# Optimization experiments

Measured on AMD Instinct MI355X. Metric: run time of the kernel, lower is better.

The kernel has to match this reference:

```python
import jax, jax.numpy as jnp
import numpy as np
import math

B, W, D, H, K = 32, 512, 512, 8, 64
DH = D // H

def _rms(x, s, eps=1e-6):
    return x / jnp.sqrt(jnp.mean(x * x, axis=-1, keepdims=True) + eps) * s

def _l2n(x):
    return x / (jnp.linalg.norm(x, axis=-1, keepdims=True) + 1e-6)

def _rope(x, fc):
    b, t, h, d = x.shape
    xc = jax.lax.complex(x[..., 0::2], x[..., 1::2])
    xr = xc * fc
    return jnp.stack([xr.real, xr.imag], axis=-1).reshape(b, t, h, d)

def setup_inputs() -> dict:
    key = jax.random.key(0)
    ks = jax.random.split(key, 24)
    n = lambda i, s: jax.random.normal(ks[i], s, jnp.float32) * 0.02
    return {
        'x': jax.random.normal(ks[0], (B, W, D), jnp.float32),
        'epi_keys': _l2n(jax.random.normal(ks[1], (B, K, D), jnp.float32)),
        'epi_vals': jax.random.normal(ks[2], (B, K, D), jnp.float32),
        'epi_age': jax.random.uniform(ks[3], (B, K), jnp.float32, 0.0, 10.0),
        'epi_strength': jax.random.uniform(ks[4], (B, K), jnp.float32, 0.01, 1.0),
        'pos_idx': jnp.arange(W, dtype=jnp.int32),
        'rms1': jnp.ones((D,), jnp.float32), 'rms_kv': jnp.ones((D,), jnp.float32),
        'rms2': jnp.ones((D,), jnp.float32), 'rms_read': jnp.ones((D,), jnp.float32),
        'Wq': n(5, (D, D)), 'bq': jnp.zeros((D,), jnp.float32),
        'Wk': n(6, (D, D)), 'bk': jnp.zeros((D,), jnp.float32),
        'Wv': n(7, (D, D)), 'bv': jnp.zeros((D,), jnp.float32),
        'Wo': n(8, (D, D)), 'bo': jnp.zeros((D,), jnp.float32),
        'W1': n(9, (D, 8 * D)), 'W2': n(10, (4 * D, D)),
        'Wwk': n(11, (D, D)), 'bwk': jnp.zeros((D,), jnp.float32),
        'Wwv': n(12, (D, D)), 'bwv': jnp.zeros((D,), jnp.float32),
        'Wws': n(13, (D, 1)), 'bws': jnp.zeros((1,), jnp.float32),
        'Wg1': n(14, (D + 2, D)), 'bg1': jnp.zeros((D,), jnp.float32),
        'Wg2': n(15, (D, 1)), 'bg2': jnp.zeros((1,), jnp.float32),
    }

def _cell(x, epi_keys, epi_vals, epi_age, epi_strength, pos_idx,
          rms1, rms_kv, rms2, rms_read, Wq, bq, Wk, bk, Wv, bv, Wo, bo,
          W1, W2, Wwk, bwk, Wwv, bwv, Wws, bws, Wg1, bg1, Wg2, bg2):
    Bc, T, Dc = x.shape
    # RoPE freqs at absolute window positions (slice_freqs_cis)
    freqs = 1.0 / (10000.0 ** (jnp.arange(0, DH, 2, dtype=jnp.float32) / DH))  # (DH/2,)
    ang = pos_idx.astype(jnp.float32)[:, None] * freqs[None, :]               # (T, DH/2)
    fc = jax.lax.complex(jnp.cos(ang), jnp.sin(ang))[None, :, None, :]        # (1,T,1,DH/2)
    # --- windowed causal RoPE attention (TransformerBlock) ---
    nx, nkv = _rms(x, rms1), _rms(x, rms_kv)
    q = _rope((nx @ Wq + bq).reshape(Bc, T, H, DH), fc)
    k = _rope((nkv @ Wk + bk).reshape(Bc, T, H, DH), fc)
    v = (nkv @ Wv + bv).reshape(Bc, T, H, DH)
    att = jnp.einsum('bthd,bshd->bhts', q, k) / math.sqrt(DH)
    causal = jnp.tril(jnp.ones((T, T), bool))
    att = jnp.where(causal[None, None], att, -1e9)
    p = jax.nn.softmax(att, axis=-1)
    o = jnp.einsum('bhts,bshd->bthd', p, v).reshape(Bc, T, Dc)
    h1 = x + (o @ Wo + bo)
    gv = _rms(h1, rms2) @ W1
    g, val = jnp.split(gv, 2, axis=-1)
    h2 = h1 + (jax.nn.silu(g) * val) @ W2                                     # (B,T,D)
    # --- window summary query ---
    q_win = jnp.mean(h2, axis=1)                                              # (B,D)
    # --- EpisodicSlotReader ---
    qn = _l2n(q_win)
    kn = _l2n(epi_keys)
    sim_r = jnp.sum(kn * qn[:, None, :], axis=-1)                             # (B,K)
    logits = sim_r + 0.5 * jnp.log(jnp.clip(epi_strength, 0.001, 1e9)) - 0.02 * epi_age
    logits = logits + ((epi_strength > 0.001).astype(jnp.float32) - 1.0) * 1000.0
    w_read = jax.nn.softmax(logits, axis=-1)
    read = _rms(jnp.sum(w_read[:, :, None] * epi_vals, axis=1), rms_read)     # (B,D)
    # --- write projections ---
    write_key = q_win @ Wwk + bwk
    write_val = q_win @ Wwv + bwv
    ws = jnp.clip(jax.nn.sigmoid(q_win @ Wws + bws), 0.0, 1.0)                # (B,1)
    # --- EpisodicSlotWriter (ST top-1 competitive write) ---
    wk_n = _l2n(write_key)
    sim_w = jnp.sum(kn * wk_n[:, None, :], axis=-1)                           # (B,K)
    soft = jax.nn.softmax(sim_w * 50.0, axis=-1)
    hard = jax.nn.one_hot(jnp.argmax(soft, axis=-1), K, dtype=jnp.float32)
    write_w = jax.lax.stop_gradient(hard - soft) + soft
    eff = write_w * ws * 0.5                                                  # (B,K)
    re = eff[:, :, None]
    keys_new = _l2n((1.0 - re) * epi_keys + re * write_key[:, None, :])
    vals_new = (1.0 - re) * epi_vals + re * write_val[:, None, :]
    age_new = (epi_age + 1.0) * (1.0 - write_w)
    sn = epi_strength * 0.995
    sn = jnp.clip(sn + write_w * ws * (1.0 - sn), 0.001, 1.0)
    best_sim = jnp.max(sim_w, axis=-1)                                        # (B,)
    # --- MemoryRecallGate ---
    novelty = (1.0 - best_sim)[:, None]
    xg = jnp.concatenate([q_win, ws, novelty], axis=-1)                       # (B,D+2)
    gate = jax.nn.sigmoid(jax.nn.silu(xg @ Wg1 + bg1) @ Wg2 + bg2)            # (B,1)
    out = h2 + (gate * read)[:, None, :]
    return out, keys_new, vals_new, age_new, sn, gate

def reference(x, epi_keys, epi_vals, epi_age, epi_strength, pos_idx,
              rms1, rms_kv, rms2, rms_read, Wq, bq, Wk, bk, Wv, bv, Wo, bo,
              W1, W2, Wwk, bwk, Wwv, bwv, Wws, bws, Wg1, bg1, Wg2, bg2):
    return _cell(x, epi_keys, epi_vals, epi_age, epi_strength, pos_idx,
                 rms1, rms_kv, rms2, rms_read, Wq, bq, Wk, bk, Wv, bv, Wo, bo,
                 W1, W2, Wwk, bwk, Wwv, bwv, Wws, bws, Wg1, bg1, Wg2, bg2)
```

## Files before the change

### kernel.cpp

```cpp
#include <hip/hip_runtime.h>


#define DEVI __device__ __forceinline__
typedef unsigned short u16;
typedef unsigned int   u32;
typedef __bf16 v8bf __attribute__((ext_vector_type(8)));
typedef float  v4f  __attribute__((ext_vector_type(4)));

DEVI float bf2f(u16 u) { u32 v = ((u32)u) << 16; return __builtin_bit_cast(float, v); }
DEVI u16 f2bf(float f) {
  u32 x = __builtin_bit_cast(u32, f);
  u32 r = x + 0x7fffu + ((x >> 16) & 1u);
  return (u16)(r >> 16);
}
DEVI uint4 pack8(const float* f) {
  u32 a[4];
#pragma unroll
  for (int i = 0; i < 4; ++i)
    a[i] = (u32)f2bf(f[2*i]) | ((u32)f2bf(f[2*i+1]) << 16);
  uint4 v; v.x = a[0]; v.y = a[1]; v.z = a[2]; v.w = a[3]; return v;
}
DEVI void ld8f(const float* p, float* f) {
  float4 a = *(const float4*)p, b = *(const float4*)(p + 4);
  f[0]=a.x; f[1]=a.y; f[2]=a.z; f[3]=a.w; f[4]=b.x; f[5]=b.y; f[6]=b.z; f[7]=b.w;
}
DEVI void st8f(float* p, const float* f) {
  *(float4*)p       = make_float4(f[0], f[1], f[2], f[3]);
  *(float4*)(p + 4) = make_float4(f[4], f[5], f[6], f[7]);
}
DEVI v8bf ldfrag(const u16* p) { return __builtin_bit_cast(v8bf, *(const uint4*)p); }

DEVI void async16(const u16* g, u16* l) {
  __builtin_amdgcn_global_load_lds(
      (const __attribute__((address_space(1))) void*)g,
      (__attribute__((address_space(3))) void*)l, 16, 0, 0);
}

DEVI float wave_sum64(float v) {
  v += __shfl_xor(v, 1);  v += __shfl_xor(v, 2);  v += __shfl_xor(v, 4);
  v += __shfl_xor(v, 8);  v += __shfl_xor(v, 16); v += __shfl_xor(v, 32);
  return v;
}

__device__ float block_sum256(float v, float* sred) {
  v = wave_sum64(v);
  int w = threadIdx.x >> 6;
  __syncthreads();
  if ((threadIdx.x & 63) == 0) sred[w] = v;
  __syncthreads();
  return sred[0] + sred[1] + sred[2] + sred[3];
}

__global__ __launch_bounds__(256) void transpose_all_k(
    const float* __restrict__ Wq, const float* __restrict__ Wk,
    const float* __restrict__ Wv, const float* __restrict__ Wo,
    const float* __restrict__ W1, const float* __restrict__ W2,
    const float* __restrict__ rms1, const float* __restrict__ rms_kv,
    const float* __restrict__ rms2, u16* __restrict__ WTqkv,
    u16* __restrict__ WTo, u16* __restrict__ WT1, u16* __restrict__ WT2,
    const float* __restrict__ bq, const float* __restrict__ bk,
    const float* __restrict__ bv, float* __restrict__ bias_qkv) {
  int id = blockIdx.x;
  if (id >= 4096) {
    int j = (id - 4096) * 256 + threadIdx.x;
    bias_qkv[j] = j < 512 ? bq[j] : (j < 1024 ? bk[j - 512] : bv[j - 1024]);
    return;
  }
  const float* in; const float* scale; u16* outp; int R, C, bx, by;
  if (id < 256)       { in=Wq; scale=rms1;   outp=WTqkv;            R=512;  C=512;  int l=id;       bx=l&15;  by=l>>4; }
  else if (id < 512)  { in=Wk; scale=rms_kv; outp=WTqkv+512*512;    R=512;  C=512;  int l=id-256;   bx=l&15;  by=l>>4; }
  else if (id < 768)  { in=Wv; scale=rms_kv; outp=WTqkv+1024*512;   R=512;  C=512;  int l=id-512;   bx=l&15;  by=l>>4; }
  else if (id < 1024) { in=Wo; scale=nullptr;outp=WTo;              R=512;  C=512;  int l=id-768;   bx=l&15;  by=l>>4; }
  else if (id < 3072) { in=W1; scale=rms2;   outp=WT1;              R=512;  C=4096; int l=id-1024;  bx=l&127; by=l>>7; }
  else                { in=W2; scale=nullptr;outp=WT2;              R=2048; C=512;  int l=id-3072;  bx=l&15;  by=l>>4; }
  __shared__ u16 t[32][33];
  int c0 = bx * 32, r0 = by * 32;
  int lc = threadIdx.x & 31, lr = threadIdx.x >> 5;
  for (int rr = lr; rr < 32; rr += 8) {
    float v = in[(size_t)(r0 + rr) * C + c0 + lc];
    if (scale) v *= scale[r0 + rr];
    t[rr][lc] = f2bf(v);
  }
  __syncthreads();
  for (int rr = lr; rr < 32; rr += 8)
    outp[(size_t)(c0 + rr) * R + r0 + lc] = t[lc][rr];
}

__global__ __launch_bounds__(256) void rms_k(const float* __restrict__ x,
                                             u16* __restrict__ o1) {
  int w = threadIdx.x >> 6, lane = threadIdx.x & 63;
  size_t row = (size_t)blockIdx.x * 4 + w;
  float xf[8]; ld8f(x + row * 512 + lane * 8, xf);
  float ss = 0.f;
#pragma unroll
  for (int i = 0; i < 8; ++i) ss += xf[i] * xf[i];
  ss = wave_sum64(ss);
  float inv = rsqrtf(ss * (1.f / 512.f) + 1e-6f);
  float of[8];
#pragma unroll
  for (int i = 0; i < 8; ++i) of[i] = xf[i] * inv;
  *(uint4*)(o1 + row * 512 + lane * 8) = pack8(of);
}

__global__ __launch_bounds__(256) void gemm128_k(const u16* __restrict__ A,
                                                 const u16* __restrict__ BT,
                                                 const float* __restrict__ bias,
                                                 const float* __restrict__ resf,
                                                 u16* __restrict__ outb,
                                                 float* __restrict__ outf,
                                                 int N, int Kd) {
  __shared__ u16 As[128 * 64];
  __shared__ u16 Bs[128 * 64];
  int tid = threadIdx.x;
  int w = tid >> 6, lane = tid & 63;
  int m = lane & 15, quad = lane >> 4;
  int wm = w >> 1, wn = w & 1;
  int bm = blockIdx.x, bn = blockIdx.y;
  v4f acc[4][4] = {};
  const int gswz = ((lane & 7) ^ (lane >> 3)) * 8;
  const u16* Ag = A + (size_t)(bm * 128 + w * 32 + (lane >> 3)) * Kd + gswz;
  const u16* Bg = BT + (size_t)(bn * 128 + w * 32 + (lane >> 3)) * Kd + gswz;
  u16* Al = &As[w * 32 * 64];
  u16* Bl = &Bs[w * 32 * 64];
  const int rsw = (m & 7) * 8;
  for (int k0 = 0; k0 < Kd; k0 += 64) {
#pragma unroll
    for (int it = 0; it < 4; ++it) {
      async16(Ag + (size_t)it * 8 * Kd + k0, Al + it * 8 * 64);
      async16(Bg + (size_t)it * 8 * Kd + k0, Bl + it * 8 * 64);
    }
    __syncthreads();
#pragma unroll
    for (int kk = 0; kk < 2; ++kk) {
      v8bf af[4], bfr[4];
#pragma unroll
      for (int i = 0; i < 4; ++i)
        af[i] = ldfrag(&As[(wm * 64 + i * 16 + m) * 64 +
                           ((kk * 32 + quad * 8) ^ rsw)]);
#pragma unroll
      for (int j = 0; j < 4; ++j)
        bfr[j] = ldfrag(&Bs[(wn * 64 + j * 16 + m) * 64 +
                            ((kk * 32 + quad * 8) ^ rsw)]);
#pragma unroll
      for (int i = 0; i < 4; ++i)
#pragma unroll
        for (int j = 0; j < 4; ++j)
          acc[i][j] = __builtin_amdgcn_mfma_f32_16x16x32_bf16(af[i], bfr[j],
                                                              acc[i][j], 0, 0, 0);
    }
    __syncthreads();
  }
#pragma unroll
  for (int i = 0; i < 4; ++i) {
    int grow0 = bm * 128 + wm * 64 + i * 16 + quad * 4;
#pragma unroll
    for (int j = 0; j < 4; ++j) {
      int gcol = bn * 128 + wn * 64 + j * 16 + m;
      float bv = bias ? bias[gcol] : 0.f;
#pragma unroll
      for (int rr = 0; rr < 4; ++rr) {
        size_t idx = (size_t)(grow0 + rr) * N + gcol;
        float v = acc[i][j][rr] + bv;
        if (resf) v += resf[idx];
        if (outb) outb[idx] = f2bf(v);
        else      outf[idx] = v;
      }
    }
  }
}

__global__ __launch_bounds__(256) void mlp1_k(const u16* __restrict__ A,
                                              const u16* __restrict__ W1T,
                                              u16* __restrict__ out) {
  __shared__ u16 As[128 * 64];
  __shared__ u16 Bgs[64 * 64];
  __shared__ u16 Bvs[64 * 64];
  const int Kd = 512;
  int tid = threadIdx.x;
  int w = tid >> 6, lane = tid & 63;
  int m = lane & 15, quad = lane >> 4;
  int bm = blockIdx.x, bn = blockIdx.y;
  v4f accg[2][4] = {}, accv[2][4] = {};
  const int gswz = ((lane & 7) ^ (lane >> 3)) * 8;
  const u16* Ag  = A + (size_t)(bm * 128 + w * 32 + (lane >> 3)) * Kd + gswz;
  const u16* Bgp = W1T + (size_t)(bn * 64 + w * 16 + (lane >> 3)) * Kd + gswz;
  const u16* Bvp = W1T + (size_t)(2048 + bn * 64 + w * 16 + (lane >> 3)) * Kd + gswz;
  u16* Al  = &As[w * 32 * 64];
  u16* Bgl = &Bgs[w * 16 * 64];
  u16* Bvl = &Bvs[w * 16 * 64];
  const int rsw = (m & 7) * 8;
  for (int k0 = 0; k0 < Kd; k0 += 64) {
#pragma unroll
    for (int it = 0; it < 4; ++it)
      async16(Ag + (size_t)it * 8 * Kd + k0, Al + it * 8 * 64);
#pragma unroll
    for (int it = 0; it < 2; ++it) {
      async16(Bgp + (size_t)it * 8 * Kd + k0, Bgl + it * 8 * 64);
      async16(Bvp + (size_t)it * 8 * Kd + k0, Bvl + it * 8 * 64);
    }
    __syncthreads();
#pragma unroll
    for (int kk = 0; kk < 2; ++kk) {
      v8bf af[2], bg[4], bv[4];
#pragma unroll
      for (int i = 0; i < 2; ++i)
        af[i] = ldfrag(&As[(w * 32 + i * 16 + m) * 64 +
                           ((kk * 32 + quad * 8) ^ rsw)]);
#pragma unroll
      for (int j = 0; j < 4; ++j) {
        bg[j] = ldfrag(&Bgs[(j * 16 + m) * 64 + ((kk * 32 + quad * 8) ^ rsw)]);
        bv[j] = ldfrag(&Bvs[(j * 16 + m) * 64 + ((kk * 32 + quad * 8) ^ rsw)]);
      }
#pragma unroll
      for (int i = 0; i < 2; ++i)
#pragma unroll
        for (int j = 0; j < 4; ++j) {
          accg[i][j] = __builtin_amdgcn_mfma_f32_16x16x32_bf16(af[i], bg[j],
                                                               accg[i][j], 0, 0, 0);
          accv[i][j] = __builtin_amdgcn_mfma_f32_16x16x32_bf16(af[i], bv[j],
                                                               accv[i][j], 0, 0, 0);
        }
    }
    __syncthreads();
  }
#pragma unroll
  for (int i = 0; i < 2; ++i) {
    int grow0 = bm * 128 + w * 32 + i * 16 + quad * 4;
#pragma unroll
    for (int j = 0; j < 4; ++j) {
      int gcol = bn * 64 + j * 16 + m;
#pragma unroll
      for (int rr = 0; rr < 4; ++rr) {
        float g = accg[i][j][rr];
        float sv = g / (1.f + __expf(-g));
        out[(size_t)(grow0 + rr) * 2048 + gcol] = f2bf(sv * accv[i][j][rr]);
      }
    }
  }
}

__global__ __launch_bounds__(256) void rope_qk_k(u16* __restrict__ qkv,
                                                 const int* __restrict__ pos) {
  int pid = blockIdx.x * 256 + threadIdx.x;
  int half = pid >> 22;
  int sub = pid & 0x3FFFFF;
  int row = sub >> 8;
  int pr = sub & 255;
  int tt = row & 511;
  int col2 = half * 512 + pr * 2;
  int f = pr & 31;
  float freq = exp2f(-0.41524101186f * (float)f);
  float ang = (float)pos[tt] * freq;
  float sv, cv;
  sincosf(ang, &sv, &cv);
  u16* p = qkv + (size_t)row * 1536 + col2;
  u32 v = *(u32*)p;
  float e = bf2f((u16)(v & 0xffffu)), o = bf2f((u16)(v >> 16));
  float ne = e * cv - o * sv;
  float no = e * sv + o * cv;
  *(u32*)p = (u32)f2bf(ne) | ((u32)f2bf(no) << 16);
}

__global__ __launch_bounds__(1024) void attn_k(const u16* __restrict__ qkv,
                                               u16* __restrict__ og) {
  __shared__ u16 Ks[512 * 64];
  __shared__ u16 Vt[64 * 512];
  __shared__ u16 Ps[16][16 * 40];
  int tid = threadIdx.x;
  int w = tid >> 6, lane = tid & 63;
  int m = lane & 15, quad = lane >> 4;
  int bh = blockIdx.x;
  int b = bh >> 3, h = bh & 7;
  const size_t qbase = (size_t)b * 512 * 1536 + h * 64;
  const size_t obase = (size_t)b * 512 * 512 + h * 64;
  const u16* kbase = qkv + (size_t)b * 512 * 1536 + 512 + h * 64;
  const u16* vbase = kbase + 512;

  {
    int d8 = (tid & 7) * 8;
    for (int s = tid >> 3; s < 512; s += 128) {
      uint4 t4 = *(const uint4*)(kbase + (size_t)s * 1536 + d8);
      *(uint4*)&Ks[s * 64 + (d8 ^ ((s & 7) * 8))] = t4;
    }
  }
  {
    int d = tid & 63, sw = (d & 7) * 8;
    for (int s = tid >> 6; s < 512; s += 16)
      Vt[d * 512 + (s ^ sw)] = vbase[(size_t)s * 1536 + d];
  }
  __syncthreads();

  for (int rep = 0; rep < 2; ++rep) {
    int qt = rep == 0 ? w : 31 - w;
    int tb = qt * 16;
    const u16* qp = qkv + qbase + (size_t)(tb + m) * 1536;
    v8bf aq0 = ldfrag(qp + quad * 8);
    v8bf aq1 = ldfrag(qp + 32 + quad * 8);
    v4f acc[4] = {};
    float mr[4], lr_[4];
#pragma unroll
    for (int rr = 0; rr < 4; ++rr) { mr[rr] = -1.0e30f; lr_[rr] = 0.f; }
    int swz = (m & 7) * 8;

    for (int st2 = 0; st2 <= qt; st2 += 2) {
      int srA = st2 * 16 + m;
      v8bf ka0 = ldfrag(&Ks[srA * 64 + ((quad * 8) ^ swz)]);
      v8bf ka1 = ldfrag(&Ks[srA * 64 + ((32 + quad * 8) ^ swz)]);
      v4f s4a = {};
      __builtin_amdgcn_s_setprio(1);
      s4a = __builtin_amdgcn_mfma_f32_16x16x32_bf16(aq0, ka0, s4a, 0, 0, 0);
      s4a = __builtin_amdgcn_mfma_f32_16x16x32_bf16(aq1, ka1, s4a, 0, 0, 0);
      __builtin_amdgcn_s_setprio(0);
      bool haveB = (st2 + 1 <= qt);
      v4f s4b = {};
      if (haveB) {
        int srB = srA + 16;
        v8bf kb0 = ldfrag(&Ks[srB * 64 + ((quad * 8) ^ swz)]);
        v8bf kb1 = ldfrag(&Ks[srB * 64 + ((32 + quad * 8) ^ swz)]);
        __builtin_amdgcn_s_setprio(1);
        s4b = __builtin_amdgcn_mfma_f32_16x16x32_bf16(aq0, kb0, s4b, 0, 0, 0);
        s4b = __builtin_amdgcn_mfma_f32_16x16x32_bf16(aq1, kb1, s4b, 0, 0, 0);
        __builtin_amdgcn_s_setprio(0);
      }
      float sca[4], scb[4];
#pragma unroll
      for (int rr = 0; rr < 4; ++rr) {
        int rowt = tb + quad * 4 + rr;
        sca[rr] = s4a[rr] * 0.125f;
        if (st2 == qt && st2 * 16 + m > rowt) sca[rr] = -1.0e9f;
        scb[rr] = haveB ? s4b[rr] * 0.125f : -1.0e30f;
        if (haveB && st2 + 1 == qt && (st2 + 1) * 16 + m > rowt) scb[rr] = -1.0e9f;
      }
      float pva[4], pvb[4], alpha[4];
#pragma unroll
      for (int rr = 0; rr < 4; ++rr) {
        float v = fmaxf(sca[rr], scb[rr]);
        v = fmaxf(v, __shfl_xor(v, 1));
        v = fmaxf(v, __shfl_xor(v, 2));
        v = fmaxf(v, __shfl_xor(v, 4));
        v = fmaxf(v, __shfl_xor(v, 8));
        float mn = fmaxf(mr[rr], v);
        alpha[rr] = __expf(mr[rr] - mn);
        pva[rr] = __expf(sca[rr] - mn);
        pvb[rr] = __expf(scb[rr] - mn);
        mr[rr] = mn;
      }
#pragma unroll
      for (int rr = 0; rr < 4; ++rr) {
        float s = pva[rr] + pvb[rr];
        s += __shfl_xor(s, 1); s += __shfl_xor(s, 2);
        s += __shfl_xor(s, 4); s += __shfl_xor(s, 8);
        lr_[rr] = lr_[rr] * alpha[rr] + s;
#pragma unroll
        for (int c = 0; c < 4; ++c) acc[c][rr] *= alpha[rr];
        Ps[w][(quad * 4 + rr) * 40 + m]      = f2bf(pva[rr]);
        Ps[w][(quad * 4 + rr) * 40 + 16 + m] = f2bf(pvb[rr]);
      }
      __asm__ volatile("" ::: "memory");
      v8bf pf = ldfrag(&Ps[w][m * 40 + quad * 8]);
      __builtin_amdgcn_s_setprio(1);
#pragma unroll
      for (int c = 0; c < 4; ++c) {
        int drow = c * 16 + m;
        v8bf vf = ldfrag(&Vt[drow * 512 +
                             ((st2 * 16 + quad * 8) ^ ((drow & 7) * 8))]);
        acc[c] = __builtin_amdgcn_mfma_f32_16x16x32_bf16(pf, vf, acc[c], 0, 0, 0);
      }
      __builtin_amdgcn_s_setprio(0);
    }
#pragma unroll
    for (int rr = 0; rr < 4; ++rr) {
      int t = tb + quad * 4 + rr;
      float inv = 1.f / lr_[rr];
      u16* op = og + obase + (size_t)t * 512;
#pragma unroll
      for (int c = 0; c < 4; ++c) op[c * 16 + m] = f2bf(acc[c][rr] * inv);
    }
  }
}

__global__ __launch_bounds__(256) void qwin_k(const float* __restrict__ h2,
                                              float* __restrict__ part) {
  int bc = blockIdx.x;
  int b = bc >> 3;
  int c = bc & 7;
  int d2 = threadIdx.x * 2;
  float a0 = 0.f, a1 = 0.f;
  for (int i = 0; i < 64; ++i) {
    int t = c * 64 + i;
    float2 v = *(const float2*)(h2 + ((size_t)(b * 512 + t)) * 512 + d2);
    a0 += v.x;
    a1 += v.y;
  }
  part[(size_t)bc * 512 + d2]     = a0;
  part[(size_t)bc * 512 + d2 + 1] = a1;
}

__global__ __launch_bounds__(256) void qw_k(const float* __restrict__ part,
                                            float* __restrict__ qw_g) {
  int b = blockIdx.x;
#pragma unroll
  for (int u = 0; u < 2; ++u) {
    int d = threadIdx.x + u * 256;
    float s = 0.f;
#pragma unroll
    for (int c = 0; c < 8; ++c) s += part[((size_t)b * 8 + c) * 512 + d];
    qw_g[(size_t)b * 512 + d] = s * (1.f / 512.f);
  }
}

__global__ __launch_bounds__(256) void gemv_k(
    const float* __restrict__ qw_g, const float* __restrict__ Wwk,
    const float* __restrict__ bwk, const float* __restrict__ Wwv,
    const float* __restrict__ bwv, const float* __restrict__ Wg1,
    const float* __restrict__ bg1, const float* __restrict__ Wws,
    const float* __restrict__ bws, float* __restrict__ wkey_g,
    float* __restrict__ wval_g, float* __restrict__ abase_g,
    float* __restrict__ ws_g) {
  __shared__ float qs[512];
  __shared__ float prt[4][64];
  __shared__ float sred[8];
  int tid = threadIdx.x;
  int b = blockIdx.y, cg = blockIdx.x;
  qs[tid]       = qw_g[(size_t)b * 512 + tid];
  qs[tid + 256] = qw_g[(size_t)b * 512 + tid + 256];
  __syncthreads();
  if (cg == 24) {
    float p = qs[tid] * Wws[tid] + qs[tid + 256] * Wws[tid + 256];
    float tot = block_sum256(p, sred);
    if (tid == 0) {
      float wsv = 1.f / (1.f + __expf(-(tot + bws[0])));
      ws_g[b] = fminf(fmaxf(wsv, 0.f), 1.f);
    }
    return;
  }
  int sel = cg >> 3;
  int c0 = (cg & 7) * 64;
  const float* W = sel == 0 ? Wwk : (sel == 1 ? Wwv : Wg1);
  const float* bias = sel == 0 ? bwk : (sel == 1 ? bwv : bg1);
  float* dst = sel == 0 ? wkey_g : (sel == 1 ? wval_g : abase_g);
  int kg = tid >> 6, cl = tid & 63;
  const float* Wp = W + (size_t)(kg * 128) * 512 + c0 + cl;
  float acc = 0.f;
#pragma unroll 8
  for (int i = 0; i < 128; ++i) acc += qs[kg * 128 + i] * Wp[(size_t)i * 512];
  prt[kg][cl] = acc;
  __syncthreads();
  if (tid < 64)
    dst[(size_t)b * 512 + c0 + tid] =
        prt[0][tid] + prt[1][tid] + prt[2][tid] + prt[3][tid] + bias[c0 + tid];
}

__global__ __launch_bounds__(256) void epi2_k(
    const float* __restrict__ qw_g, const float* __restrict__ wkey_g,
    const float* __restrict__ wval_g, const float* __restrict__ abase_g,
    const float* __restrict__ ws_g, const float* __restrict__ keys,
    const float* __restrict__ vals, const float* __restrict__ age,
    const float* __restrict__ strength, const float* __restrict__ Wg1,
    const float* __restrict__ Wg2, const float* __restrict__ bg2,
    const float* __restrict__ rms_read, float* __restrict__ read_f,
    float* __restrict__ gate_f, float* __restrict__ keys_out,
    float* __restrict__ vals_out, float* __restrict__ age_out,
    float* __restrict__ sn_out, float* __restrict__ gate_out) {
  int b = blockIdx.x;
  int tid = threadIdx.x;
  int w = tid >> 6, lane = tid & 63;
  __shared__ float qs[512], wkl[512], wvl[512];
  __shared__ float knorm[64], sr[64], swv[64], wread[64];
  __shared__ float sred[8];
  __shared__ float scal[2];
  __shared__ int bestk;
  __shared__ float novs;

  qs[tid]        = qw_g[(size_t)b * 512 + tid];
  qs[tid + 256]  = qw_g[(size_t)b * 512 + tid + 256];
  wkl[tid]       = wkey_g[(size_t)b * 512 + tid];
  wkl[tid + 256] = wkey_g[(size_t)b * 512 + tid + 256];
  wvl[tid]       = wval_g[(size_t)b * 512 + tid];
  wvl[tid + 256] = wval_g[(size_t)b * 512 + tid + 256];
  __syncthreads();
  float ws_s = ws_g[b];
  float p = qs[tid] * qs[tid] + qs[tid + 256] * qs[tid + 256];
  float tot = block_sum256(p, sred);
  if (tid == 0) scal[0] = 1.f / (sqrtf(tot) + 1e-6f);
  p = wkl[tid] * wkl[tid] + wkl[tid + 256] * wkl[tid + 256];
  tot = block_sum256(p, sred);
  if (tid == 0) scal[1] = 1.f / (sqrtf(tot) + 1e-6f);
  __syncthreads();
  float qscale = scal[0], wscale = scal[1];
  for (int k = w; k < 64; k += 4) {
    float kf[8];
    ld8f(keys + ((size_t)b * 64 + k) * 512 + lane * 8, kf);
    float s2 = 0.f, sq = 0.f, sw = 0.f;
#pragma unroll
    for (int i = 0; i < 8; ++i) {
      s2 += kf[i] * kf[i];
      sq += kf[i] * qs[lane * 8 + i];
      sw += kf[i] * wkl[lane * 8 + i];
    }
    s2 = wave_sum64(s2);
    sq = wave_sum64(sq);
    sw = wave_sum64(sw);
    if (lane == 0) {
      float kn = sqrtf(s2) + 1e-6f;
      knorm[k] = kn;
      float st = strength[b * 64 + k];
      float ag = age[b * 64 + k];
      sr[k] = (sq * qscale) / kn + 0.5f * logf(fminf(fmaxf(st, 0.001f), 1e9f)) -
              0.02f * ag + ((st > 0.001f) ? 0.f : -1000.f);
      swv[k] = (sw * wscale) / kn;
    }
  }
  __syncthreads();
  if (w == 0) {
    float v = sr[lane];
    float mx = v;
    mx = fmaxf(mx, __shfl_xor(mx, 1));  mx = fmaxf(mx, __shfl_xor(mx, 2));
    mx = fmaxf(mx, __shfl_xor(mx, 4));  mx = fmaxf(mx, __shfl_xor(mx, 8));
    mx = fmaxf(mx, __shfl_xor(mx, 16)); mx = fmaxf(mx, __shfl_xor(mx, 32));
    float e = __expf(v - mx);
    float sm = wave_sum64(e);
    wread[lane] = e / sm;
  } else if (w == 1) {
    float v = swv[lane];
    int idx = lane;
#pragma unroll
    for (int mm = 1; mm < 64; mm <<= 1) {
      float ov = __shfl_xor(v, mm);
      int oi = __shfl_xor(idx, mm);
      if (ov > v || (ov == v && oi < idx)) { v = ov; idx = oi; }
    }
    if (lane == 0) { bestk = idx; novs = 1.f - v; }
  }
  __syncthreads();
  float rv0 = 0.f, rv1 = 0.f;
  for (int k = 0; k < 64; ++k) {
    float wr = wread[k];
    const float* vp = vals + ((size_t)b * 64 + k) * 512;
    rv0 += wr * vp[tid];
    rv1 += wr * vp[tid + 256];
  }
  p = rv0 * rv0 + rv1 * rv1;
  tot = block_sum256(p, sred);
  float rinv = rsqrtf(tot * (1.f / 512.f) + 1e-6f);
  read_f[(size_t)b * 512 + tid]       = rv0 * rinv * rms_read[tid];
  read_f[(size_t)b * 512 + tid + 256] = rv1 * rinv * rms_read[tid + 256];
  if (tid < 64) {
    int k = tid;
    float hard = (k == bestk) ? 1.f : 0.f;
    float ag = age[b * 64 + k];
    age_out[b * 64 + k] = (ag + 1.f) * (1.f - hard);
    float st = strength[b * 64 + k];
    float s0 = st * 0.995f;
    float snv = s0 + hard * ws_s * (1.f - s0);
    sn_out[b * 64 + k] = fminf(fmaxf(snv, 0.001f), 1.f);
  }
  for (int k = w; k < 64; k += 4) {
    float re = (k == bestk) ? ws_s * 0.5f : 0.f;
    float kf[8], vf[8];
    ld8f(keys + ((size_t)b * 64 + k) * 512 + lane * 8, kf);
    ld8f(vals + ((size_t)b * 64 + k) * 512 + lane * 8, vf);
    float u[8], ss = 0.f;
#pragma unroll
    for (int i = 0; i < 8; ++i) {
      u[i] = (1.f - re) * kf[i] + re * wkl[lane * 8 + i];
      ss += u[i] * u[i];
    }
    ss = wave_sum64(ss);
    float uinv = 1.f / (sqrtf(ss) + 1e-6f);
    float ko[8], vo[8];
#pragma unroll
    for (int i = 0; i < 8; ++i) {
      ko[i] = u[i] * uinv;
      vo[i] = (1.f - re) * vf[i] + re * wvl[lane * 8 + i];
    }
    st8f(keys_out + ((size_t)b * 64 + k) * 512 + lane * 8, ko);
    st8f(vals_out + ((size_t)b * 64 + k) * 512 + lane * 8, vo);
  }
  __syncthreads();
  float nov = novs;
  float a0 = abase_g[(size_t)b * 512 + tid] +
             ws_s * Wg1[(size_t)512 * 512 + tid] +
             nov * Wg1[(size_t)513 * 512 + tid];
  float a1 = abase_g[(size_t)b * 512 + tid + 256] +
             ws_s * Wg1[(size_t)512 * 512 + tid + 256] +
             nov * Wg1[(size_t)513 * 512 + tid + 256];
  float h0 = a0 / (1.f + __expf(-a0));
  float h1v = a1 / (1.f + __expf(-a1));
  float gp = h0 * Wg2[tid] + h1v * Wg2[tid + 256];
  tot = block_sum256(gp, sred);
  if (tid == 0) {
    float g = 1.f / (1.f + __expf(-(tot + bg2[0])));
    gate_f[b] = g;
    gate_out[b] = g;
  }
}

__global__ __launch_bounds__(256) void final_k(const float* __restrict__ h2,
                                               const float* __restrict__ read_f,
                                               const float* __restrict__ gate_f,
                                               float* __restrict__ outp) {
  size_t i2 = ((size_t)blockIdx.x * 256 + threadIdx.x) * 2;
  int b = (int)(i2 >> 18);
  int d = (int)(i2 & 511);
  float g = gate_f[b];
  float2 h = *(const float2*)(h2 + i2);
  outp[i2]     = h.x + g * read_f[b * 512 + d];
  outp[i2 + 1] = h.y + g * read_f[b * 512 + d + 1];
}

extern "C" void kernel_launch(void* const* d_in, const int* in_sizes, int n_in,
                              void* d_out, int out_size, void* d_ws,
                              size_t ws_size, hipStream_t stream) {
  const float* x        = (const float*)d_in[0];
  const float* epi_keys = (const float*)d_in[1];
  const float* epi_vals = (const float*)d_in[2];
  const float* epi_age  = (const float*)d_in[3];
  const float* epi_str  = (const float*)d_in[4];
  const int*   pos      = (const int*)d_in[5];
  const float* rms1     = (const float*)d_in[6];
  const float* rms_kv   = (const float*)d_in[7];
  const float* rms2     = (const float*)d_in[8];
  const float* rms_read = (const float*)d_in[9];
  const float* Wq = (const float*)d_in[10]; const float* bq = (const float*)d_in[11];
  const float* Wk = (const float*)d_in[12]; const float* bk = (const float*)d_in[13];
  const float* Wv = (const float*)d_in[14]; const float* bv = (const float*)d_in[15];
  const float* Wo = (const float*)d_in[16]; const float* bo = (const float*)d_in[17];
  const float* W1 = (const float*)d_in[18]; const float* W2 = (const float*)d_in[19];
  const float* Wwk = (const float*)d_in[20]; const float* bwk = (const float*)d_in[21];
  const float* Wwv = (const float*)d_in[22]; const float* bwv = (const float*)d_in[23];
  const float* Wws = (const float*)d_in[24]; const float* bws = (const float*)d_in[25];
  const float* Wg1 = (const float*)d_in[26]; const float* bg1 = (const float*)d_in[27];
  const float* Wg2 = (const float*)d_in[28]; const float* bg2 = (const float*)d_in[29];

  float* out      = (float*)d_out;
  float* out_main = out;
  float* out_keys = out + 8388608;
  float* out_vals = out + 9437184;
  float* out_age  = out + 10485760;
  float* out_sn   = out + 10487808;
  float* out_gate = out + 10489856;

  char* w8 = (char*)d_ws;
  size_t off = 0;
  auto alloc = [&](size_t bytes) {
    char* pp = w8 + off;
    off += (bytes + 255) & ~(size_t)255;
    return pp;
  };
  u16* WTqkv = (u16*)alloc((size_t)1536 * 512 * 2);
  u16* WTo   = (u16*)alloc(512 * 512 * 2);
  u16* WT1   = (u16*)alloc((size_t)4096 * 512 * 2);
  u16* WT2   = (u16*)alloc((size_t)512 * 2048 * 2);
  const size_t TB = (size_t)16384 * 512 * 2;
  u16* nrm  = (u16*)alloc(TB);
  u16* qkvb = (u16*)alloc(3 * TB);
  u16* ob   = (u16*)alloc(TB);
  u16* n2   = (u16*)alloc(TB);
  float* h1f = (float*)alloc((size_t)16384 * 512 * 4);
  u16*   gact = nrm;
  float* h2f  = (float*)ob;
  float* bias_qkv = (float*)alloc(1536 * 4);
  float* part    = (float*)alloc((size_t)32 * 8 * 512 * 4);
  float* qw_g    = (float*)alloc((size_t)32 * 512 * 4);
  float* wkey_g  = (float*)alloc((size_t)32 * 512 * 4);
  float* wval_g  = (float*)alloc((size_t)32 * 512 * 4);
  float* abase_g = (float*)alloc((size_t)32 * 512 * 4);
  float* ws_g    = (float*)alloc(64 * 4);
  float* read_f  = (float*)alloc((size_t)32 * 512 * 4);
  float* gate_f  = (float*)alloc(64 * 4);

  transpose_all_k<<<4102, 256, 0, stream>>>(Wq, Wk, Wv, Wo, W1, W2, rms1,
                                            rms_kv, rms2, WTqkv, WTo, WT1,
                                            WT2, bq, bk, bv, bias_qkv);
  rms_k<<<4096, 256, 0, stream>>>(x, nrm);
  gemm128_k<<<dim3(128, 12), 256, 0, stream>>>(nrm, WTqkv, bias_qkv, nullptr,
                                               qkvb, nullptr, 1536, 512);
  rope_qk_k<<<32768, 256, 0, stream>>>(qkvb, pos);
  attn_k<<<256, 1024, 0, stream>>>(qkvb, ob);
  gemm128_k<<<dim3(128, 4), 256, 0, stream>>>(ob, WTo, bo, x,
                                              nullptr, h1f, 512, 512);
  rms_k<<<4096, 256, 0, stream>>>(h1f, n2);
  mlp1_k<<<dim3(128, 32), 256, 0, stream>>>(n2, WT1, gact);
  gemm128_k<<<dim3(128, 4), 256, 0, stream>>>(gact, WT2, nullptr, h1f,
                                              nullptr, h2f, 512, 2048);
  qwin_k<<<256, 256, 0, stream>>>(h2f, part);
  qw_k<<<32, 256, 0, stream>>>(part, qw_g);
  gemv_k<<<dim3(25, 32), 256, 0, stream>>>(qw_g, Wwk, bwk, Wwv, bwv, Wg1, bg1,
                                           Wws, bws, wkey_g, wval_g, abase_g, ws_g);
  epi2_k<<<32, 256, 0, stream>>>(qw_g, wkey_g, wval_g, abase_g, ws_g, epi_keys,
                                 epi_vals, epi_age, epi_str, Wg1, Wg2, bg2,
                                 rms_read, read_f, gate_f, out_keys, out_vals,
                                 out_age, out_sn, out_gate);
  final_k<<<16384, 256, 0, stream>>>(h2f, read_f, gate_f, out_main);
}
```

Measured before the change: 516.4 us.

## Fuse RoPE into attention loads and merge prep, rms, and qw reduction kernels

Removes the standalone RoPE kernel, which did a read-modify-write over all Q and K columns. A cos/sin table is now precomputed per position in a merged prep kernel, and the rotation is applied to Q and K as attention loads them. The first RMS norm and the zeroing of qw_g also move into the prep kernel. The two-stage qw reduction becomes one kernel using float atomics. This saves several launches and a full pass over the QKV buffer, but atomics make the reduction order nondeterministic and attention does a little more work per load.

```diff
diff --git a/kernel.cpp b/kernel.cpp
--- a/kernel.cpp
+++ b/kernel.cpp
@@ -30,6 +30,13 @@
 }
 DEVI v8bf ldfrag(const u16* p) { return __builtin_bit_cast(v8bf, *(const uint4*)p); }
 
+DEVI u32 rot1(u32 w, float c, float s) {
+  float e = bf2f((u16)(w & 0xffffu)), o = bf2f((u16)(w >> 16));
+  float ne = e * c - o * s;
+  float no = e * s + o * c;
+  return (u32)f2bf(ne) | ((u32)f2bf(no) << 16);
+}
+
 DEVI void async16(const u16* g, u16* l) {
   __builtin_amdgcn_global_load_lds(
       (const __attribute__((address_space(1))) void*)g,
@@ -51,7 +58,7 @@
   return sred[0] + sred[1] + sred[2] + sred[3];
 }
 
-__global__ __launch_bounds__(256) void transpose_all_k(
+__global__ __launch_bounds__(256) void prep_k(
     const float* __restrict__ Wq, const float* __restrict__ Wk,
     const float* __restrict__ Wv, const float* __restrict__ Wo,
     const float* __restrict__ W1, const float* __restrict__ W2,
@@ -59,10 +66,44 @@
     const float* __restrict__ rms2, u16* __restrict__ WTqkv,
     u16* __restrict__ WTo, u16* __restrict__ WT1, u16* __restrict__ WT2,
     const float* __restrict__ bq, const float* __restrict__ bk,
-    const float* __restrict__ bv, float* __restrict__ bias_qkv) {
+    const float* __restrict__ bv, float* __restrict__ bias_qkv,
+    const int* __restrict__ pos, float* __restrict__ tbl,
+    float* __restrict__ qw_g, const float* __restrict__ x,
+    u16* __restrict__ nrm) {
   int id = blockIdx.x;
+  int tid = threadIdx.x;
+  if (id >= 4230) {
+    int w = tid >> 6, lane = tid & 63;
+    size_t row = (size_t)(id - 4230) * 4 + w;
+    float xf[8]; ld8f(x + row * 512 + lane * 8, xf);
+    float ss = 0.f;
+#pragma unroll
+    for (int i = 0; i < 8; ++i) ss += xf[i] * xf[i];
+    ss = wave_sum64(ss);
+    float inv = rsqrtf(ss * (1.f / 512.f) + 1e-6f);
+    float of[8];
+#pragma unroll
+    for (int i = 0; i < 8; ++i) of[i] = xf[i] * inv;
+    *(uint4*)(nrm + row * 512 + lane * 8) = pack8(of);
+    return;
+  }
+  if (id >= 4166) {
+    qw_g[(id - 4166) * 256 + tid] = 0.f;
+    return;
+  }
+  if (id >= 4102) {
+    int idx = (id - 4102) * 256 + tid;
+    int t = idx >> 5, f = idx & 31;
+    float freq = exp2f(-0.41524101186f * (float)f);
+    float ang = (float)pos[t] * freq;
+    float sv, cv;
+    sincosf(ang, &sv, &cv);
+    tbl[t * 64 + f * 2]     = cv;
+    tbl[t * 64 + f * 2 + 1] = sv;
+    return;
+  }
   if (id >= 4096) {
-    int j = (id - 4096) * 256 + threadIdx.x;
+    int j = (id - 4096) * 256 + tid;
     bias_qkv[j] = j < 512 ? bq[j] : (j < 1024 ? bk[j - 512] : bv[j - 1024]);
     return;
   }
@@ -75,7 +116,7 @@
   else                { in=W2; scale=nullptr;outp=WT2;              R=2048; C=512;  int l=id-3072;  bx=l&15;  by=l>>4; }
   __shared__ u16 t[32][33];
   int c0 = bx * 32, r0 = by * 32;
-  int lc = threadIdx.x & 31, lr = threadIdx.x >> 5;
+  int lc = tid & 31, lr = tid >> 5;
   for (int rr = lr; rr < 32; rr += 8) {
     float v = in[(size_t)(r0 + rr) * C + c0 + lc];
     if (scale) v *= scale[r0 + rr];
@@ -239,29 +280,8 @@
   }
 }
 
-__global__ __launch_bounds__(256) void rope_qk_k(u16* __restrict__ qkv,
-                                                 const int* __restrict__ pos) {
-  int pid = blockIdx.x * 256 + threadIdx.x;
-  int half = pid >> 22;
-  int sub = pid & 0x3FFFFF;
-  int row = sub >> 8;
-  int pr = sub & 255;
-  int tt = row & 511;
-  int col2 = half * 512 + pr * 2;
-  int f = pr & 31;
-  float freq = exp2f(-0.41524101186f * (float)f);
-  float ang = (float)pos[tt] * freq;
-  float sv, cv;
-  sincosf(ang, &sv, &cv);
-  u16* p = qkv + (size_t)row * 1536 + col2;
-  u32 v = *(u32*)p;
-  float e = bf2f((u16)(v & 0xffffu)), o = bf2f((u16)(v >> 16));
-  float ne = e * cv - o * sv;
-  float no = e * sv + o * cv;
-  *(u32*)p = (u32)f2bf(ne) | ((u32)f2bf(no) << 16);
-}
-
 __global__ __launch_bounds__(1024) void attn_k(const u16* __restrict__ qkv,
+                                               const float* __restrict__ tbl,
                                                u16* __restrict__ og) {
   __shared__ u16 Ks[512 * 64];
   __shared__ u16 Vt[64 * 512];
@@ -280,6 +300,12 @@
     int d8 = (tid & 7) * 8;
     for (int s = tid >> 3; s < 512; s += 128) {
       uint4 t4 = *(const uint4*)(kbase + (size_t)s * 1536 + d8);
+      const float4* tp = (const float4*)(tbl + s * 64 + d8);
+      float4 cs01 = tp[0], cs23 = tp[1];
+      t4.x = rot1(t4.x, cs01.x, cs01.y);
+      t4.y = rot1(t4.y, cs01.z, cs01.w);
+      t4.z = rot1(t4.z, cs23.x, cs23.y);
+      t4.w = rot1(t4.w, cs23.z, cs23.w);
       *(uint4*)&Ks[s * 64 + (d8 ^ ((s & 7) * 8))] = t4;
     }
   }
@@ -294,8 +320,21 @@
     int qt = rep == 0 ? w : 31 - w;
     int tb = qt * 16;
     const u16* qp = qkv + qbase + (size_t)(tb + m) * 1536;
-    v8bf aq0 = ldfrag(qp + quad * 8);
-    v8bf aq1 = ldfrag(qp + 32 + quad * 8);
+    uint4 q0 = *(const uint4*)(qp + quad * 8);
+    uint4 q1 = *(const uint4*)(qp + 32 + quad * 8);
+    {
+      const float* tq = tbl + (tb + m) * 64;
+      float4 a = *(const float4*)(tq + quad * 8);
+      float4 b4 = *(const float4*)(tq + quad * 8 + 4);
+      q0.x = rot1(q0.x, a.x, a.y);   q0.y = rot1(q0.y, a.z, a.w);
+      q0.z = rot1(q0.z, b4.x, b4.y); q0.w = rot1(q0.w, b4.z, b4.w);
+      float4 c4 = *(const float4*)(tq + 32 + quad * 8);
+      float4 d4 = *(const float4*)(tq + 36 + quad * 8);
+      q1.x = rot1(q1.x, c4.x, c4.y); q1.y = rot1(q1.y, c4.z, c4.w);
+      q1.z = rot1(q1.z, d4.x, d4.y); q1.w = rot1(q1.w, d4.z, d4.w);
+    }
+    v8bf aq0 = __builtin_bit_cast(v8bf, q0);
+    v8bf aq1 = __builtin_bit_cast(v8bf, q1);
     v4f acc[4] = {};
     float mr[4], lr_[4];
 #pragma unroll
@@ -379,8 +418,8 @@
   }
 }
 
-__global__ __launch_bounds__(256) void qwin_k(const float* __restrict__ h2,
-                                              float* __restrict__ part) {
+__global__ __launch_bounds__(256) void qwsum_k(const float* __restrict__ h2,
+                                               float* __restrict__ qw_g) {
   int bc = blockIdx.x;
   int b = bc >> 3;
   int c = bc & 7;
@@ -392,21 +431,8 @@
     a0 += v.x;
     a1 += v.y;
   }
-  part[(size_t)bc * 512 + d2]     = a0;
-  part[(size_t)bc * 512 + d2 + 1] = a1;
-}
-
-__global__ __launch_bounds__(256) void qw_k(const float* __restrict__ part,
-                                            float* __restrict__ qw_g) {
-  int b = blockIdx.x;
-#pragma unroll
-  for (int u = 0; u < 2; ++u) {
-    int d = threadIdx.x + u * 256;
-    float s = 0.f;
-#pragma unroll
-    for (int c = 0; c < 8; ++c) s += part[((size_t)b * 8 + c) * 512 + d];
-    qw_g[(size_t)b * 512 + d] = s * (1.f / 512.f);
-  }
+  atomicAdd(qw_g + (size_t)b * 512 + d2,     a0 * (1.f / 512.f));
+  atomicAdd(qw_g + (size_t)b * 512 + d2 + 1, a1 * (1.f / 512.f));
 }
 
 __global__ __launch_bounds__(256) void gemv_k(
@@ -661,7 +687,7 @@
   u16*   gact = nrm;
   float* h2f  = (float*)ob;
   float* bias_qkv = (float*)alloc(1536 * 4);
-  float* part    = (float*)alloc((size_t)32 * 8 * 512 * 4);
+  float* tbl      = (float*)alloc((size_t)512 * 64 * 4);
   float* qw_g    = (float*)alloc((size_t)32 * 512 * 4);
   float* wkey_g  = (float*)alloc((size_t)32 * 512 * 4);
   float* wval_g  = (float*)alloc((size_t)32 * 512 * 4);
@@ -670,22 +696,19 @@
   float* read_f  = (float*)alloc((size_t)32 * 512 * 4);
   float* gate_f  = (float*)alloc(64 * 4);
 
-  transpose_all_k<<<4102, 256, 0, stream>>>(Wq, Wk, Wv, Wo, W1, W2, rms1,
-                                            rms_kv, rms2, WTqkv, WTo, WT1,
-                                            WT2, bq, bk, bv, bias_qkv);
-  rms_k<<<4096, 256, 0, stream>>>(x, nrm);
+  prep_k<<<8326, 256, 0, stream>>>(Wq, Wk, Wv, Wo, W1, W2, rms1, rms_kv, rms2,
+                                   WTqkv, WTo, WT1, WT2, bq, bk, bv, bias_qkv,
+                                   pos, tbl, qw_g, x, nrm);
   gemm128_k<<<dim3(128, 12), 256, 0, stream>>>(nrm, WTqkv, bias_qkv, nullptr,
                                                qkvb, nullptr, 1536, 512);
-  rope_qk_k<<<32768, 256, 0, stream>>>(qkvb, pos);
-  attn_k<<<256, 1024, 0, stream>>>(qkvb, ob);
+  attn_k<<<256, 1024, 0, stream>>>(qkvb, tbl, ob);
   gemm128_k<<<dim3(128, 4), 256, 0, stream>>>(ob, WTo, bo, x,
                                               nullptr, h1f, 512, 512);
   rms_k<<<4096, 256, 0, stream>>>(h1f, n2);
   mlp1_k<<<dim3(128, 32), 256, 0, stream>>>(n2, WT1, gact);
   gemm128_k<<<dim3(128, 4), 256, 0, stream>>>(gact, WT2, nullptr, h1f,
                                               nullptr, h2f, 512, 2048);
-  qwin_k<<<256, 256, 0, stream>>>(h2f, part);
-  qw_k<<<32, 256, 0, stream>>>(part, qw_g);
+  qwsum_k<<<256, 256, 0, stream>>>(h2f, qw_g);
   gemv_k<<<dim3(25, 32), 256, 0, stream>>>(qw_g, Wwk, bwk, Wwv, bwv, Wg1, bg1,
                                            Wws, bws, wkey_g, wval_g, abase_g, ws_g);
   epi2_k<<<32, 256, 0, stream>>>(qw_g, wkey_g, wval_g, abase_g, ws_g, epi_keys,
```

Result: faster. 497.2 us (-3.7%).
